# Kernel optimization log

Hardware: AMD Instinct MI355X
Metric: run time of the kernel (lower is better)

The kernel has to match this reference:

```python
import jax, jax.numpy as jnp
import numpy as np

VOCAB = 32000
HID = 1024
BATCH = 8
SEQ = 512


def setup_inputs() -> dict:
    key = jax.random.key(0)
    k1, k2, k3, k4 = jax.random.split(key, 4)
    scale = 1.0 / np.sqrt(HID)
    return {
        "batched_sequence_ids": jax.random.randint(k1, (BATCH, SEQ), 0, VOCAB, dtype=jnp.int32),
        "w_out": jax.random.normal(k2, (HID, VOCAB), dtype=jnp.float32) * scale,
        "b_out": jnp.zeros((VOCAB,), dtype=jnp.float32),
        "W_ih": jax.random.normal(k3, (HID, 4 * HID), dtype=jnp.float32) * scale,
        "W_hh": jax.random.normal(k4, (HID, 4 * HID), dtype=jnp.float32) * scale,
        "b_lstm": jnp.zeros((4 * HID,), dtype=jnp.float32),
    }


def _lstm_scan(x_gates, W_hh):
    # x_gates: [B, S, 4H] = precomputed input contribution + bias
    B = x_gates.shape[0]
    H = W_hh.shape[0]
    h0 = jnp.zeros((B, H), dtype=x_gates.dtype)
    c0 = jnp.zeros((B, H), dtype=x_gates.dtype)

    def step(carry, xg_t):
        h, c = carry
        gates = xg_t + h @ W_hh  # [B, 4H]
        i, f, g, o = jnp.split(gates, 4, axis=-1)
        i = jax.nn.sigmoid(i)
        f = jax.nn.sigmoid(f)
        g = jnp.tanh(g)
        o = jax.nn.sigmoid(o)
        c_new = f * c + i * g
        h_new = o * jnp.tanh(c_new)
        return (h_new, c_new), h_new

    # scan over time axis: move S to leading dim
    (_, _), hs = jax.lax.scan(step, (h0, c0), jnp.swapaxes(x_gates, 0, 1))
    return jnp.swapaxes(hs, 0, 1)  # [B, S, H]


def reference(batched_sequence_ids, w_out, b_out, W_ih, W_hh, b_lstm):
    # weight-tied embedding lookup: w_out is [H, V]; emb = w_out[:, ids].T
    emb = jnp.take(w_out.T, batched_sequence_ids, axis=0)  # [B, S, H]
    # precompute input-to-gate contribution for all timesteps in one GEMM
    x_gates = jnp.einsum('bsh,hg->bsg', emb, W_ih) + b_lstm  # [B, S, 4H]
    hs = _lstm_scan(x_gates, W_hh)  # [B, S, H]
    logits = jnp.einsum('bsh,hv->bsv', hs, w_out) + b_out  # [B, S, V]
    return logits
```

## Files before the change

### kernel.cpp

```cpp
#include <hip/hip_runtime.h>
#include <math.h>

#define VOCAB 32000
#define HID   1024
#define BATCH 8
#define SEQ   512
#define GD    (4*HID)
#define ROWS  (BATCH*SEQ)

typedef __attribute__((ext_vector_type(8))) short short8;
typedef __attribute__((ext_vector_type(4))) float f32x4;

__device__ __forceinline__ float hi_f32(float x) {
    return __uint_as_float(__float_as_uint(x) & 0xFFFF0000u);
}
__device__ __forceinline__ unsigned pack_pair(float x) {
    unsigned hb = __float_as_uint(x) & 0xFFFF0000u;
    float lo = x - __uint_as_float(hb);
    return hb | (__float_as_uint(lo) >> 16);
}

__global__ __launch_bounds__(256) void k_gather_split(const int* __restrict__ ids,
                                                      const float* __restrict__ w_out,
                                                      unsigned short* __restrict__ emb_hi,
                                                      unsigned short* __restrict__ emb_lo)
{
    int row = blockIdx.x;
    int id  = ids[row];
    const float* src = w_out + id;
    for (int h = threadIdx.x; h < HID; h += 256) {
        float v  = src[(size_t)h * VOCAB];
        float hi = hi_f32(v);
        float lo = v - hi;
        emb_hi[(size_t)row*HID + h] = (unsigned short)(__float_as_uint(v)  >> 16);
        emb_lo[(size_t)row*HID + h] = (unsigned short)(__float_as_uint(lo) >> 16);
    }
}

__global__ __launch_bounds__(256) void k_transpose(const float* __restrict__ W,
                                                   float* __restrict__ WT)
{
    __shared__ float tile[32][33];
    int bx = blockIdx.x;
    int by = blockIdx.y;
    int x = bx*32 + threadIdx.x;
    int y = by*32 + threadIdx.y;
    #pragma unroll
    for (int i = 0; i < 32; i += 8)
        tile[threadIdx.y + i][threadIdx.x] = W[(size_t)(y + i)*GD + x];
    __syncthreads();
    int k   = by*32 + threadIdx.x;
    int col = bx*32 + threadIdx.y;
    #pragma unroll
    for (int i = 0; i < 32; i += 8)
        WT[(size_t)(col + i)*HID + k] = tile[threadIdx.x][threadIdx.y + i];
}

__global__ __launch_bounds__(256) void k_pack_pairs(const float* __restrict__ src,
                                                    unsigned int* __restrict__ dst,
                                                    long n4)
{
    long i0 = (long)blockIdx.x * 256 + threadIdx.x;
    long stride = (long)gridDim.x * 256;
    for (long i = i0; i < n4; i += stride) {
        float4 v = ((const float4*)src)[i];
        uint4 o;
        o.x = pack_pair(v.x); o.y = pack_pair(v.y);
        o.z = pack_pair(v.z); o.w = pack_pair(v.w);
        ((uint4*)dst)[i] = o;
    }
}

__global__ __launch_bounds__(256) void k_split_f32(const float* __restrict__ src,
                                                   unsigned short* __restrict__ hi,
                                                   unsigned short* __restrict__ lo,
                                                   long n4)
{
    long i0 = (long)blockIdx.x * 256 + threadIdx.x;
    long stride = (long)gridDim.x * 256;
    for (long i = i0; i < n4; i += stride) {
        float4 v = ((const float4*)src)[i];
        unsigned h0 = __float_as_uint(v.x) >> 16, h1 = __float_as_uint(v.y) >> 16;
        unsigned h2 = __float_as_uint(v.z) >> 16, h3 = __float_as_uint(v.w) >> 16;
        unsigned l0 = __float_as_uint(v.x - hi_f32(v.x)) >> 16;
        unsigned l1 = __float_as_uint(v.y - hi_f32(v.y)) >> 16;
        unsigned l2 = __float_as_uint(v.z - hi_f32(v.z)) >> 16;
        unsigned l3 = __float_as_uint(v.w - hi_f32(v.w)) >> 16;
        ((uint2*)hi)[i] = make_uint2(h0 | (h1 << 16), h2 | (h3 << 16));
        ((uint2*)lo)[i] = make_uint2(l0 | (l1 << 16), l2 | (l3 << 16));
    }
}

#define GBM 128
#define GBN 128
#define GBK 32

__global__ __launch_bounds__(256) void k_gemm_pre(const unsigned short* __restrict__ Ah,
                                                  const unsigned short* __restrict__ Al,
                                                  const unsigned int* __restrict__ Bpk,
                                                  const float* __restrict__ bias,
                                                  float* __restrict__ C,
                                                  int M, int N, int K)
{
    __shared__ unsigned short As_hi[GBM][40];
    __shared__ unsigned short As_lo[GBM][40];
    __shared__ unsigned int   Bs[GBK][132];

    int tid  = threadIdx.x;
    int brow = blockIdx.y * GBM;
    int bcol = blockIdx.x * GBN;

    int lane = tid & 63;
    int wid  = tid >> 6;
    int wm   = wid >> 1;
    int wn   = wid & 1;
    int l15  = lane & 15;
    int l4   = lane >> 4;

    int a_m = tid >> 3;
    int a_c = tid & 7;
    int b_k = tid >> 5;
    int b_n = tid & 31;

    f32x4 acc[4][4] = {};

    for (int k0 = 0; k0 < K; k0 += GBK) {
        #pragma unroll
        for (int p = 0; p < 4; ++p) {
            int r = a_m + p*32;
            *(uint2*)&As_hi[r][a_c*4] =
                *(const uint2*)(Ah + (size_t)(brow + r)*K + k0 + a_c*4);
            *(uint2*)&As_lo[r][a_c*4] =
                *(const uint2*)(Al + (size_t)(brow + r)*K + k0 + a_c*4);
        }
        #pragma unroll
        for (int p = 0; p < 4; ++p) {
            int kk = b_k + p*8;
            *(uint4*)&Bs[kk][b_n*4] =
                *(const uint4*)(Bpk + (size_t)(k0 + kk)*N + bcol + b_n*4);
        }
        __syncthreads();

        short8 ah[4], al[4];
        #pragma unroll
        for (int m = 0; m < 4; ++m) {
            int r = wm*64 + m*16 + l15;
            ah[m] = *(const short8*)&As_hi[r][l4*8];
            al[m] = *(const short8*)&As_lo[r][l4*8];
        }

        #pragma unroll
        for (int n = 0; n < 4; ++n) {
            int col = wn*64 + n*16 + l15;
            unsigned w[8];
            #pragma unroll
            for (int j = 0; j < 8; ++j)
                w[j] = Bs[l4*8 + j][col];
            union { short8 v; unsigned d[4]; } bh, bl;
            #pragma unroll
            for (int d = 0; d < 4; ++d) {
                bh.d[d] = (w[2*d] >> 16)      | (w[2*d+1] & 0xFFFF0000u);
                bl.d[d] = (w[2*d] & 0xFFFFu)  | (w[2*d+1] << 16);
            }
            #pragma unroll
            for (int m = 0; m < 4; ++m) {
                acc[m][n] = __builtin_amdgcn_mfma_f32_16x16x32_bf16(ah[m], bh.v, acc[m][n], 0, 0, 0);
                acc[m][n] = __builtin_amdgcn_mfma_f32_16x16x32_bf16(ah[m], bl.v, acc[m][n], 0, 0, 0);
                acc[m][n] = __builtin_amdgcn_mfma_f32_16x16x32_bf16(al[m], bh.v, acc[m][n], 0, 0, 0);
            }
        }
        __syncthreads();
    }

    #pragma unroll
    for (int n = 0; n < 4; ++n) {
        int col = bcol + wn*64 + n*16 + l15;
        float bv = bias[col];
        #pragma unroll
        for (int m = 0; m < 4; ++m) {
            int rb = brow + wm*64 + m*16 + l4*4;
            #pragma unroll
            for (int r = 0; r < 4; ++r)
                C[(size_t)(rb + r)*N + col] = acc[m][n][r] + bv;
        }
    }
}

__device__ __forceinline__ unsigned pack_hi2(float x, float y) {
    return (__float_as_uint(x) >> 16) | (__float_as_uint(y) & 0xFFFF0000u);
}

__global__ __launch_bounds__(256) void k_gemm_mfma(const float* __restrict__ A,
                                                   const float* __restrict__ B,
                                                   const float* __restrict__ bias,
                                                   float* __restrict__ C,
                                                   int M, int N, int K)
{
    __shared__ unsigned short As_hi[GBM][40];
    __shared__ unsigned short As_lo[GBM][40];
    __shared__ unsigned int   Bs[GBK][130];

    int tid  = threadIdx.x;
    int brow = blockIdx.y * GBM;
    int bcol = blockIdx.x * GBN;

    int lane = tid & 63;
    int wid  = tid >> 6;
    int wm   = wid >> 1;
    int wn   = wid & 1;
    int l15  = lane & 15;
    int l4   = lane >> 4;

    int a_m = tid >> 3;
    int a_c = tid & 7;
    int b_k = tid >> 5;
    int b_n = tid & 31;

    f32x4 acc[4][4] = {};

    for (int k0 = 0; k0 < K; k0 += GBK) {
        #pragma unroll
        for (int p = 0; p < 4; ++p) {
            int r = a_m + p*32;
            float4 v = *(const float4*)(A + (size_t)(brow + r)*K + k0 + a_c*4);
            unsigned h0 = pack_hi2(v.x, v.y);
            unsigned h1 = pack_hi2(v.z, v.w);
            float lx = v.x - hi_f32(v.x);
            float ly = v.y - hi_f32(v.y);
            float lz = v.z - hi_f32(v.z);
            float lw = v.w - hi_f32(v.w);
            unsigned l0 = pack_hi2(lx, ly);
            unsigned l1 = pack_hi2(lz, lw);
            *(uint2*)&As_hi[r][a_c*4] = make_uint2(h0, h1);
            *(uint2*)&As_lo[r][a_c*4] = make_uint2(l0, l1);
        }
        #pragma unroll
        for (int p = 0; p < 4; ++p) {
            int kk = b_k + p*8;
            float4 v = *(const float4*)(B + (size_t)(k0 + kk)*N + bcol + b_n*4);
            unsigned w0 = pack_pair(v.x);
            unsigned w1 = pack_pair(v.y);
            unsigned w2 = pack_pair(v.z);
            unsigned w3 = pack_pair(v.w);
            *(uint2*)&Bs[kk][b_n*4]     = make_uint2(w0, w1);
            *(uint2*)&Bs[kk][b_n*4 + 2] = make_uint2(w2, w3);
        }
        __syncthreads();

        short8 ah[4], al[4];
        #pragma unroll
        for (int m = 0; m < 4; ++m) {
            int r = wm*64 + m*16 + l15;
            ah[m] = *(const short8*)&As_hi[r][l4*8];
            al[m] = *(const short8*)&As_lo[r][l4*8];
        }

        #pragma unroll
        for (int n = 0; n < 4; ++n) {
            int col = wn*64 + n*16 + l15;
            unsigned w[8];
            #pragma unroll
            for (int j = 0; j < 8; ++j)
                w[j] = Bs[l4*8 + j][col];
            union { short8 v; unsigned d[4]; } bh, bl;
            #pragma unroll
            for (int d = 0; d < 4; ++d) {
                bh.d[d] = (w[2*d] >> 16)      | (w[2*d+1] & 0xFFFF0000u);
                bl.d[d] = (w[2*d] & 0xFFFFu)  | (w[2*d+1] << 16);
            }
            #pragma unroll
            for (int m = 0; m < 4; ++m) {
                acc[m][n] = __builtin_amdgcn_mfma_f32_16x16x32_bf16(ah[m], bh.v, acc[m][n], 0, 0, 0);
                acc[m][n] = __builtin_amdgcn_mfma_f32_16x16x32_bf16(ah[m], bl.v, acc[m][n], 0, 0, 0);
                acc[m][n] = __builtin_amdgcn_mfma_f32_16x16x32_bf16(al[m], bh.v, acc[m][n], 0, 0, 0);
            }
        }
        __syncthreads();
    }

    #pragma unroll
    for (int n = 0; n < 4; ++n) {
        int col = bcol + wn*64 + n*16 + l15;
        float bv = bias[col];
        #pragma unroll
        for (int m = 0; m < 4; ++m) {
            int rb = brow + wm*64 + m*16 + l4*4;
            #pragma unroll
            for (int r = 0; r < 4; ++r)
                C[(size_t)(rb + r)*N + col] = acc[m][n][r] + bv;
        }
    }
}

__global__ __launch_bounds__(256) void k_lstm_step(const float* __restrict__ xg,
                                                   const float* __restrict__ WT,
                                                   float* __restrict__ c_state,
                                                   float* __restrict__ hs,
                                                   int t)
{
    int j    = blockIdx.x;
    int gate = threadIdx.x >> 6;
    int lane = threadIdx.x & 63;
    int col  = gate*HID + j;

    float acc[8] = {};
    if (t > 0) {
        const float4* wv = (const float4*)(WT + (size_t)col*HID);
        #pragma unroll
        for (int c = 0; c < 4; ++c) {
            int k4 = c*64 + lane;
            float4 w4 = wv[k4];
            #pragma unroll
            for (int b = 0; b < 8; ++b) {
                float4 h4 = ((const float4*)(hs + ((size_t)b*SEQ + (t-1))*HID))[k4];
                acc[b] += w4.x*h4.x + w4.y*h4.y + w4.z*h4.z + w4.w*h4.w;
            }
        }
        #pragma unroll
        for (int b = 0; b < 8; ++b) {
            acc[b] += __shfl_xor(acc[b], 32);
            acc[b] += __shfl_xor(acc[b], 16);
            acc[b] += __shfl_xor(acc[b], 8);
            acc[b] += __shfl_xor(acc[b], 4);
            acc[b] += __shfl_xor(acc[b], 2);
            acc[b] += __shfl_xor(acc[b], 1);
        }
    }

    __shared__ float g_sm[4][8];
    if (lane == 0) {
        #pragma unroll
        for (int b = 0; b < 8; ++b)
            g_sm[gate][b] = acc[b];
    }
    __syncthreads();

    if (threadIdx.x < 8) {
        int b = threadIdx.x;
        size_t xbase = ((size_t)b*SEQ + t)*GD + j;
        float iv = g_sm[0][b] + xg[xbase];
        float fv = g_sm[1][b] + xg[xbase + HID];
        float gv = g_sm[2][b] + xg[xbase + 2*HID];
        float ov = g_sm[3][b] + xg[xbase + 3*HID];
        iv = 1.0f / (1.0f + expf(-iv));
        fv = 1.0f / (1.0f + expf(-fv));
        gv = tanhf(gv);
        ov = 1.0f / (1.0f + expf(-ov));
        float c  = (t > 0) ? c_state[(size_t)b*HID + j] : 0.0f;
        float cn = fv*c + iv*gv;
        float hn = ov * tanhf(cn);
        c_state[(size_t)b*HID + j] = cn;
        hs[((size_t)b*SEQ + t)*HID + j] = hn;
    }
}

extern "C" void kernel_launch(void* const* d_in, const int* in_sizes, int n_in,
                              void* d_out, int out_size, void* d_ws, size_t ws_size,
                              hipStream_t stream)
{
    const int*   ids    = (const int*)  d_in[0];
    const float* w_out  = (const float*)d_in[1];
    const float* b_out  = (const float*)d_in[2];
    const float* W_ih   = (const float*)d_in[3];
    const float* W_hh   = (const float*)d_in[4];
    const float* b_lstm = (const float*)d_in[5];
    float* out = (float*)d_out;

    char* ob = (char*)d_out;
    unsigned short* emb_hi = (unsigned short*)(ob);
    unsigned short* emb_lo = (unsigned short*)(ob + 8388608);
    float*          WT     = (float*)(ob + 16777216);
    float*          xg     = (float*)(ob + 33554432);
    float*          cstate = (float*)(ob + 100663296);
    unsigned int*   wih_pk = (unsigned int*)(ob + 100696064);

    char* wb = (char*)d_ws;
    float* hs = (float*)wb;
    const size_t NEED = 16777216ull + 8388608ull*2 + (size_t)VOCAB*HID*4ull;
    const bool big_ws = (ws_size >= NEED);
    unsigned short* hs_hi = (unsigned short*)(wb + 16777216);
    unsigned short* hs_lo = (unsigned short*)(wb + 25165824);
    unsigned int*   wo_pk = (unsigned int*)(wb + 33554432);

    k_gather_split<<<ROWS, 256, 0, stream>>>(ids, w_out, emb_hi, emb_lo);

    k_transpose<<<dim3(GD/32, HID/32), dim3(32, 8), 0, stream>>>(W_hh, WT);

    k_pack_pairs<<<1024, 256, 0, stream>>>(W_ih, wih_pk, (long)HID*GD/4);

    k_gemm_pre<<<dim3(GD/GBN, ROWS/GBM), 256, 0, stream>>>(
        emb_hi, emb_lo, wih_pk, b_lstm, xg, ROWS, GD, HID);

    for (int t = 0; t < SEQ; ++t)
        k_lstm_step<<<HID, 256, 0, stream>>>(xg, WT, cstate, hs, t);

    if (big_ws) {
        k_pack_pairs<<<2048, 256, 0, stream>>>(w_out, wo_pk, (long)HID*VOCAB/4);
        k_split_f32<<<1024, 256, 0, stream>>>(hs, hs_hi, hs_lo, (long)ROWS*HID/4);
        k_gemm_pre<<<dim3(VOCAB/GBN, ROWS/GBM), 256, 0, stream>>>(
            hs_hi, hs_lo, wo_pk, b_out, out, ROWS, VOCAB, HID);
    } else {
        k_gemm_mfma<<<dim3(VOCAB/GBN, ROWS/GBM), 256, 0, stream>>>(
            hs, w_out, b_out, out, ROWS, VOCAB, HID);
    }
}
```

Baseline: 5.313 ms.

## Pre-transpose GEMM weights into hi/lo bf16 and load tiles via global_load_lds

Replaces the packed hi/lo pair layout for the B operand with separate K-contiguous transposed bf16 hi and lo arrays, built by a new transpose-and-split kernel. The GEMM now copies A and B tiles straight from global memory into LDS with global_load_lds, using an XOR-swizzled layout. This removes the per-iteration register unpacking of packed B words and the strided B reads from LDS. The trade-off is an extra transposed copy of w_out, a rearranged workspace with a smaller size requirement, and the hidden-state buffer relocated into spare space in the output buffer.

New measurement: 5.221 ms. Within noise of the previous version (-1.7%).

```diff
diff --git a/kernel.cpp b/kernel.cpp
--- a/kernel.cpp
+++ b/kernel.cpp
@@ -19,6 +19,15 @@
     float lo = x - __uint_as_float(hb);
     return hb | (__float_as_uint(lo) >> 16);
 }
+__device__ __forceinline__ unsigned pack_hi2(float x, float y) {
+    return (__float_as_uint(x) >> 16) | (__float_as_uint(y) & 0xFFFF0000u);
+}
+
+__device__ __forceinline__ void gload16(const void* g, void* l) {
+    __builtin_amdgcn_global_load_lds(
+        (__attribute__((address_space(1))) void*)g,
+        (__attribute__((address_space(3))) void*)l, 16, 0, 0);
+}
 
 __global__ __launch_bounds__(256) void k_gather_split(const int* __restrict__ ids,
                                                       const float* __restrict__ w_out,
@@ -30,8 +39,7 @@
     const float* src = w_out + id;
     for (int h = threadIdx.x; h < HID; h += 256) {
         float v  = src[(size_t)h * VOCAB];
-        float hi = hi_f32(v);
-        float lo = v - hi;
+        float lo = v - hi_f32(v);
         emb_hi[(size_t)row*HID + h] = (unsigned short)(__float_as_uint(v)  >> 16);
         emb_lo[(size_t)row*HID + h] = (unsigned short)(__float_as_uint(lo) >> 16);
     }
@@ -41,33 +49,41 @@
                                                    float* __restrict__ WT)
 {
     __shared__ float tile[32][33];
-    int bx = blockIdx.x;
-    int by = blockIdx.y;
-    int x = bx*32 + threadIdx.x;
-    int y = by*32 + threadIdx.y;
+    int tx = threadIdx.x, ty = threadIdx.y;
+    int x = blockIdx.x*32 + tx;
+    int y = blockIdx.y*32 + ty;
     #pragma unroll
     for (int i = 0; i < 32; i += 8)
-        tile[threadIdx.y + i][threadIdx.x] = W[(size_t)(y + i)*GD + x];
+        tile[ty + i][tx] = W[(size_t)(y + i)*GD + x];
     __syncthreads();
-    int k   = by*32 + threadIdx.x;
-    int col = bx*32 + threadIdx.y;
+    int k   = blockIdx.y*32 + tx;
+    int col = blockIdx.x*32 + ty;
     #pragma unroll
     for (int i = 0; i < 32; i += 8)
-        WT[(size_t)(col + i)*HID + k] = tile[threadIdx.x][threadIdx.y + i];
-}
-
-__global__ __launch_bounds__(256) void k_pack_pairs(const float* __restrict__ src,
-                                                    unsigned int* __restrict__ dst,
-                                                    long n4)
-{
-    long i0 = (long)blockIdx.x * 256 + threadIdx.x;
-    long stride = (long)gridDim.x * 256;
-    for (long i = i0; i < n4; i += stride) {
-        float4 v = ((const float4*)src)[i];
-        uint4 o;
-        o.x = pack_pair(v.x); o.y = pack_pair(v.y);
-        o.z = pack_pair(v.z); o.w = pack_pair(v.w);
-        ((uint4*)dst)[i] = o;
+        WT[(size_t)(col + i)*HID + k] = tile[tx][ty + i];
+}
+
+__global__ __launch_bounds__(256) void k_transsplit(const float* __restrict__ W,
+                                                    unsigned short* __restrict__ hiT,
+                                                    unsigned short* __restrict__ loT,
+                                                    int N)
+{
+    __shared__ float tile[32][33];
+    int tx = threadIdx.x, ty = threadIdx.y;
+    int x = blockIdx.x*32 + tx;
+    int y = blockIdx.y*32 + ty;
+    #pragma unroll
+    for (int i = 0; i < 32; i += 8)
+        tile[ty + i][tx] = W[(size_t)(y + i)*N + x];
+    __syncthreads();
+    int n = blockIdx.x*32 + ty;
+    int k = blockIdx.y*32 + tx;
+    #pragma unroll
+    for (int i = 0; i < 32; i += 8) {
+        float v  = tile[tx][ty + i];
+        float lo = v - hi_f32(v);
+        hiT[(size_t)(n + i)*HID + k] = (unsigned short)(__float_as_uint(v)  >> 16);
+        loT[(size_t)(n + i)*HID + k] = (unsigned short)(__float_as_uint(lo) >> 16);
     }
 }
 
@@ -95,80 +111,73 @@
 #define GBN 128
 #define GBK 32
 
-__global__ __launch_bounds__(256) void k_gemm_pre(const unsigned short* __restrict__ Ah,
-                                                  const unsigned short* __restrict__ Al,
-                                                  const unsigned int* __restrict__ Bpk,
-                                                  const float* __restrict__ bias,
-                                                  float* __restrict__ C,
-                                                  int M, int N, int K)
-{
-    __shared__ unsigned short As_hi[GBM][40];
-    __shared__ unsigned short As_lo[GBM][40];
-    __shared__ unsigned int   Bs[GBK][132];
-
-    int tid  = threadIdx.x;
-    int brow = blockIdx.y * GBM;
-    int bcol = blockIdx.x * GBN;
-
-    int lane = tid & 63;
-    int wid  = tid >> 6;
-    int wm   = wid >> 1;
-    int wn   = wid & 1;
-    int l15  = lane & 15;
-    int l4   = lane >> 4;
-
-    int a_m = tid >> 3;
-    int a_c = tid & 7;
-    int b_k = tid >> 5;
-    int b_n = tid & 31;
+__global__ __launch_bounds__(256) void k_gemm_fast(
+    const unsigned short* __restrict__ Ah,  const unsigned short* __restrict__ Al,
+    const unsigned short* __restrict__ BhT, const unsigned short* __restrict__ BlT,
+    const float* __restrict__ bias, float* __restrict__ C,
+    int M, int N, int K)
+{
+    __shared__ __align__(16) unsigned short lds[4][4096];
+
+    const int tid  = threadIdx.x;
+    const int lane = tid & 63;
+    const int wid  = tid >> 6;
+    const int wm = wid >> 1, wn = wid & 1;
+    const int l15 = lane & 15, l4 = lane >> 4;
+    const int brow = blockIdx.y * GBM;
+    const int bcol = blockIdx.x * GBN;
+
+    const int lhi  = lane >> 3;
+    const int c8   = (lane & 7) ^ lhi;
+    const int koff = (c8 & 3) * 8;
+    const int r0   = 32*wid + 2*lhi + (c8 >> 2);
+    const int r1   = r0 + 16;
+    const size_t a0 = (size_t)(brow + r0)*K + koff;
+    const size_t a1 = (size_t)(brow + r1)*K + koff;
+    const size_t b0 = (size_t)(bcol + r0)*K + koff;
+    const size_t b1 = (size_t)(bcol + r1)*K + koff;
+    char* lbase = (char*)&lds[0][0];
+    const int cb0 = wid*2048, cb1 = wid*2048 + 1024;
+
+    const int ra = wm*64 + l15;
+    const int ga = ra >> 1;
+    const int abyte = ga*128 + (((((ra & 1) << 2) | l4) ^ (ga & 7)) << 4);
+    const int rb = wn*64 + l15;
+    const int gb = rb >> 1;
+    const int bbyte = gb*128 + (((((rb & 1) << 2) | l4) ^ (gb & 7)) << 4);
 
     f32x4 acc[4][4] = {};
 
     for (int k0 = 0; k0 < K; k0 += GBK) {
-        #pragma unroll
-        for (int p = 0; p < 4; ++p) {
-            int r = a_m + p*32;
-            *(uint2*)&As_hi[r][a_c*4] =
-                *(const uint2*)(Ah + (size_t)(brow + r)*K + k0 + a_c*4);
-            *(uint2*)&As_lo[r][a_c*4] =
-                *(const uint2*)(Al + (size_t)(brow + r)*K + k0 + a_c*4);
-        }
-        #pragma unroll
-        for (int p = 0; p < 4; ++p) {
-            int kk = b_k + p*8;
-            *(uint4*)&Bs[kk][b_n*4] =
-                *(const uint4*)(Bpk + (size_t)(k0 + kk)*N + bcol + b_n*4);
-        }
+        gload16(Ah  + a0 + k0, lbase         + cb0);
+        gload16(Ah  + a1 + k0, lbase         + cb1);
+        gload16(Al  + a0 + k0, lbase + 8192  + cb0);
+        gload16(Al  + a1 + k0, lbase + 8192  + cb1);
+        gload16(BhT + b0 + k0, lbase + 16384 + cb0);
+        gload16(BhT + b1 + k0, lbase + 16384 + cb1);
+        gload16(BlT + b0 + k0, lbase + 24576 + cb0);
+        gload16(BlT + b1 + k0, lbase + 24576 + cb1);
         __syncthreads();
 
-        short8 ah[4], al[4];
+        short8 ah[4], al[4], bh[4], bl[4];
         #pragma unroll
         for (int m = 0; m < 4; ++m) {
-            int r = wm*64 + m*16 + l15;
-            ah[m] = *(const short8*)&As_hi[r][l4*8];
-            al[m] = *(const short8*)&As_lo[r][l4*8];
-        }
-
+            ah[m] = *(const short8*)(lbase         + abyte + m*1024);
+            al[m] = *(const short8*)(lbase + 8192  + abyte + m*1024);
+        }
         #pragma unroll
         for (int n = 0; n < 4; ++n) {
-            int col = wn*64 + n*16 + l15;
-            unsigned w[8];
-            #pragma unroll
-            for (int j = 0; j < 8; ++j)
-                w[j] = Bs[l4*8 + j][col];
-            union { short8 v; unsigned d[4]; } bh, bl;
-            #pragma unroll
-            for (int d = 0; d < 4; ++d) {
-                bh.d[d] = (w[2*d] >> 16)      | (w[2*d+1] & 0xFFFF0000u);
-                bl.d[d] = (w[2*d] & 0xFFFFu)  | (w[2*d+1] << 16);
+            bh[n] = *(const short8*)(lbase + 16384 + bbyte + n*1024);
+            bl[n] = *(const short8*)(lbase + 24576 + bbyte + n*1024);
+        }
+        #pragma unroll
+        for (int n = 0; n < 4; ++n)
+            #pragma unroll
+            for (int m = 0; m < 4; ++m) {
+                acc[m][n] = __builtin_amdgcn_mfma_f32_16x16x32_bf16(ah[m], bh[n], acc[m][n], 0, 0, 0);
+                acc[m][n] = __builtin_amdgcn_mfma_f32_16x16x32_bf16(ah[m], bl[n], acc[m][n], 0, 0, 0);
+                acc[m][n] = __builtin_amdgcn_mfma_f32_16x16x32_bf16(al[m], bh[n], acc[m][n], 0, 0, 0);
             }
-            #pragma unroll
-            for (int m = 0; m < 4; ++m) {
-                acc[m][n] = __builtin_amdgcn_mfma_f32_16x16x32_bf16(ah[m], bh.v, acc[m][n], 0, 0, 0);
-                acc[m][n] = __builtin_amdgcn_mfma_f32_16x16x32_bf16(ah[m], bl.v, acc[m][n], 0, 0, 0);
-                acc[m][n] = __builtin_amdgcn_mfma_f32_16x16x32_bf16(al[m], bh.v, acc[m][n], 0, 0, 0);
-            }
-        }
         __syncthreads();
     }
 
@@ -178,16 +187,12 @@
         float bv = bias[col];
         #pragma unroll
         for (int m = 0; m < 4; ++m) {
-            int rb = brow + wm*64 + m*16 + l4*4;
+            int rbs = brow + wm*64 + m*16 + l4*4;
             #pragma unroll
             for (int r = 0; r < 4; ++r)
-                C[(size_t)(rb + r)*N + col] = acc[m][n][r] + bv;
-        }
-    }
-}
-
-__device__ __forceinline__ unsigned pack_hi2(float x, float y) {
-    return (__float_as_uint(x) >> 16) | (__float_as_uint(y) & 0xFFFF0000u);
+                C[(size_t)(rbs + r)*N + col] = acc[m][n][r] + bv;
+        }
+    }
 }
 
 __global__ __launch_bounds__(256) void k_gemm_mfma(const float* __restrict__ A,
@@ -367,38 +372,43 @@
     float* out = (float*)d_out;
 
     char* ob = (char*)d_out;
-    unsigned short* emb_hi = (unsigned short*)(ob);
-    unsigned short* emb_lo = (unsigned short*)(ob + 8388608);
-    float*          WT     = (float*)(ob + 16777216);
-    float*          xg     = (float*)(ob + 33554432);
-    float*          cstate = (float*)(ob + 100663296);
-    unsigned int*   wih_pk = (unsigned int*)(ob + 100696064);
+    unsigned short* emb_hi  = (unsigned short*)(ob);
+    unsigned short* emb_lo  = (unsigned short*)(ob + 8388608);
+    float*          WT      = (float*)(ob + 16777216);
+    float*          xg      = (float*)(ob + 33554432);
+    float*          cstate  = (float*)(ob + 100663296);
+    unsigned short* wih_hiT = (unsigned short*)(ob + 100696064);
+    unsigned short* wih_loT = (unsigned short*)(ob + 109084672);
+    float*          hs_dout = (float*)(ob + 117473280);
 
     char* wb = (char*)d_ws;
-    float* hs = (float*)wb;
-    const size_t NEED = 16777216ull + 8388608ull*2 + (size_t)VOCAB*HID*4ull;
+    const size_t NEED = 147849216ull;
     const bool big_ws = (ws_size >= NEED);
-    unsigned short* hs_hi = (unsigned short*)(wb + 16777216);
-    unsigned short* hs_lo = (unsigned short*)(wb + 25165824);
-    unsigned int*   wo_pk = (unsigned int*)(wb + 33554432);
+    unsigned short* hs_hi  = (unsigned short*)(wb);
+    unsigned short* hs_lo  = (unsigned short*)(wb + 8388608);
+    unsigned short* wo_hiT = (unsigned short*)(wb + 16777216);
+    unsigned short* wo_loT = (unsigned short*)(wb + 82313216);
+    float* hs = big_ws ? hs_dout : (float*)wb;
 
     k_gather_split<<<ROWS, 256, 0, stream>>>(ids, w_out, emb_hi, emb_lo);
 
     k_transpose<<<dim3(GD/32, HID/32), dim3(32, 8), 0, stream>>>(W_hh, WT);
 
-    k_pack_pairs<<<1024, 256, 0, stream>>>(W_ih, wih_pk, (long)HID*GD/4);
-
-    k_gemm_pre<<<dim3(GD/GBN, ROWS/GBM), 256, 0, stream>>>(
-        emb_hi, emb_lo, wih_pk, b_lstm, xg, ROWS, GD, HID);
+    k_transsplit<<<dim3(GD/32, HID/32), dim3(32, 8), 0, stream>>>(
+        W_ih, wih_hiT, wih_loT, GD);
+
+    k_gemm_fast<<<dim3(GD/GBN, ROWS/GBM), 256, 0, stream>>>(
+        emb_hi, emb_lo, wih_hiT, wih_loT, b_lstm, xg, ROWS, GD, HID);
 
     for (int t = 0; t < SEQ; ++t)
         k_lstm_step<<<HID, 256, 0, stream>>>(xg, WT, cstate, hs, t);
 
     if (big_ws) {
-        k_pack_pairs<<<2048, 256, 0, stream>>>(w_out, wo_pk, (long)HID*VOCAB/4);
+        k_transsplit<<<dim3(VOCAB/32, HID/32), dim3(32, 8), 0, stream>>>(
+            w_out, wo_hiT, wo_loT, VOCAB);
         k_split_f32<<<1024, 256, 0, stream>>>(hs, hs_hi, hs_lo, (long)ROWS*HID/4);
-        k_gemm_pre<<<dim3(VOCAB/GBN, ROWS/GBM), 256, 0, stream>>>(
-            hs_hi, hs_lo, wo_pk, b_out, out, ROWS, VOCAB, HID);
+        k_gemm_fast<<<dim3(VOCAB/GBN, ROWS/GBM), 256, 0, stream>>>(
+            hs_hi, hs_lo, wo_hiT, wo_loT, b_out, out, ROWS, VOCAB, HID);
     } else {
         k_gemm_mfma<<<dim3(VOCAB/GBN, ROWS/GBM), 256, 0, stream>>>(
             hs, w_out, b_out, out, ROWS, VOCAB, HID);
```
